# Optimization experiments

Hardware: AMD Instinct MI355X
Metric: run time of the kernel (lower is better)

Reference implementation:

```python
import jax, jax.numpy as jnp
import numpy as np

N_NODES = 50000
IN_CH = 128
OUT_CH = 64
HID = 2 * OUT_CH  # 128
N_EDGES = 800000


def _glorot(key, shape):
    fan_in, fan_out = shape[0], shape[-1]
    lim = jnp.sqrt(6.0 / (fan_in + fan_out))
    return jax.random.uniform(key, shape, jnp.float32, -lim, lim)


def setup_inputs() -> dict:
    key = jax.random.key(0)
    ks = jax.random.split(key, 10)
    x = jax.random.normal(ks[0], (N_NODES, IN_CH), jnp.float32)
    edge_index = jax.random.randint(ks[1], (2, N_EDGES), 0, N_NODES, jnp.int32)
    return {
        "x": x,
        "edge_index": edge_index,
        "W1": _glorot(ks[2], (IN_CH, HID)),
        "a_src1": _glorot(ks[3], (HID,)),
        "a_dst1": _glorot(ks[4], (HID,)),
        "b1": jnp.zeros((HID,), jnp.float32),
        "W2": _glorot(ks[5], (HID, OUT_CH)),
        "a_src2": _glorot(ks[6], (OUT_CH,)),
        "a_dst2": _glorot(ks[7], (OUT_CH,)),
        "b2": jnp.zeros((OUT_CH,), jnp.float32),
    }


def _gat_conv(x, src, dst, W, a_src, a_dst, b, n_nodes):
    # Linear transform: [N, F_out]
    h = x @ W
    # Per-node attention halves (heads=1): alpha_i = <h_i, a>
    al_s = h @ a_src  # [N]
    al_d = h @ a_dst  # [N]
    # Edge scores with LeakyReLU(0.2), PyG default negative slope
    e = jax.nn.leaky_relu(al_s[src] + al_d[dst], negative_slope=0.2)
    # Segment softmax over incoming edges of each dst node
    m = jax.ops.segment_max(e, dst, num_segments=n_nodes)
    m = jnp.where(jnp.isfinite(m), m, 0.0)
    ex = jnp.exp(e - m[dst])
    denom = jax.ops.segment_sum(ex, dst, num_segments=n_nodes)
    alpha = ex / (denom[dst] + 1e-16)  # [E]
    # Weighted scatter-add aggregation
    out = jax.ops.segment_sum(h[src] * alpha[:, None], dst, num_segments=n_nodes)
    return out + b


def reference(x, edge_index, W1, a_src1, a_dst1, b1, W2, a_src2, a_dst2, b2):
    n = x.shape[0]
    # add_self_loops=True (PyG GATConv default)
    loops = jnp.arange(n, dtype=edge_index.dtype)
    src = jnp.concatenate([edge_index[0], loops])
    dst = jnp.concatenate([edge_index[1], loops])
    h = _gat_conv(x.astype(jnp.float32), src, dst, W1, a_src1, a_dst1, b1, n)
    h = jax.nn.relu(h)
    return _gat_conv(h, src, dst, W2, a_src2, a_dst2, b2, n)
```

## Files before the change

### kernel.cpp

```cpp
#include <hip/hip_runtime.h>
#include <hip/hip_bf16.h>

#define N_NODES 50000
#define IN_CH 128
#define HID 128
#define OUT_CH 64
#define N_EDGES 800000
#define N_TOT_EDGES (N_EDGES + N_NODES)
#define ET_PAD (N_TOT_EDGES + 3 * N_NODES)
#define MPAD 50048
#define NBX (MPAD / 16)
#define NBN ((N_NODES + 255) / 256)

typedef float float4v __attribute__((ext_vector_type(4)));
typedef unsigned uint4v __attribute__((ext_vector_type(4)));
typedef __attribute__((ext_vector_type(8))) short bf16x8;
typedef __attribute__((ext_vector_type(4))) float f32x4;

__device__ __forceinline__ unsigned bf16_rne(float f) {
    unsigned u = __float_as_uint(f);
    return (u + 0x7fffu + ((u >> 16) & 1u)) >> 16;
}
__device__ __forceinline__ unsigned pack2(float a, float b) {
    return bf16_rne(a) | (bf16_rne(b) << 16);
}


__global__ void k_count(const int* __restrict__ dst_row, int* __restrict__ cnt,
                        unsigned short* __restrict__ rank, int e) {
    int i = blockIdx.x * 256 + threadIdx.x;
    if (i < e) {
        int d = __builtin_nontemporal_load(&dst_row[i]);
        rank[i] = (unsigned short)atomicAdd(&cnt[d], 1);
    }
}

__global__ void k_scan1(const int* __restrict__ cnt, int* __restrict__ off,
                        int* __restrict__ bsum, int n) {
    __shared__ int s[256];
    int t = threadIdx.x;
    int i = blockIdx.x * 256 + t;
    int v = (i < n) ? ((cnt[i] + 3) & ~3) : 0;
    s[t] = v;
    __syncthreads();
    for (int d = 1; d < 256; d <<= 1) {
        int x = (t >= d) ? s[t - d] : 0;
        __syncthreads();
        s[t] += x;
        __syncthreads();
    }
    if (i < n) off[i + 1] = s[t];
    if (t == 255) bsum[blockIdx.x] = s[255];
}

__global__ void k_scan2(int* __restrict__ bsum, int nb) {
    __shared__ int s[256];
    int t = threadIdx.x;
    int v = (t < nb) ? bsum[t] : 0;
    s[t] = v;
    __syncthreads();
    for (int d = 1; d < 256; d <<= 1) {
        int x = (t >= d) ? s[t - d] : 0;
        __syncthreads();
        s[t] += x;
        __syncthreads();
    }
    if (t < nb) bsum[t] = s[t] - v;
}

__global__ void k_scan3(int* __restrict__ off, const int* __restrict__ bsum, int n) {
    int i = blockIdx.x * 256 + threadIdx.x;
    if (i < n) off[i + 1] += bsum[blockIdx.x];
    if (i == 0) off[0] = 0;
}

__global__ void k_fill2(const int* __restrict__ ei, const int* __restrict__ off,
                        const unsigned short* __restrict__ rank,
                        int* __restrict__ csr, int e, int n) {
    int i = blockIdx.x * 256 + threadIdx.x;
    if (i < e) {
        int src = __builtin_nontemporal_load(&ei[i]);
        int dst = __builtin_nontemporal_load(&ei[e + i]);
        csr[off[dst] + rank[i]] = src;
    } else if (i < e + n) {
        int v = i - e;
        csr[off[v]] = v;
    }
}

__global__ __launch_bounds__(256) void k_cvtAll(
        const float* __restrict__ X, unsigned short* __restrict__ Xb,
        const float* __restrict__ W1, unsigned short* __restrict__ Wl1,
        const float* __restrict__ W2, unsigned short* __restrict__ Wl2,
        int* __restrict__ cnt, int M) {
    const int b = blockIdx.x;
    const int t = threadIdx.x;
    if (b < NBX) {
        const int kg = t >> 4, rl = t & 15;
        const int row = b * 16 + rl;
        float4 a = make_float4(0.f, 0.f, 0.f, 0.f), c = a;
        if (row < M) {
            a = *(const float4*)&X[(size_t)row * 128 + kg * 8];
            c = *(const float4*)&X[(size_t)row * 128 + kg * 8 + 4];
        }
        uint4 p;
        p.x = pack2(a.x, a.y); p.y = pack2(a.z, a.w);
        p.z = pack2(c.x, c.y); p.w = pack2(c.z, c.w);
        *(uint4*)&Xb[(size_t)b * 2048 + kg * 128 + rl * 8] = p;
        return;
    }
    if (b >= NBX + 12) {
        int i = (b - NBX - 12) * 256 + t;
        if (i < M) cnt[i] = 1;
        return;
    }
    const float* W; unsigned short* Wl; int N, bb;
    if (b < NBX + 8) { W = W1; Wl = Wl1; N = 128; bb = b - NBX; }
    else             { W = W2; Wl = Wl2; N = 64;  bb = b - NBX - 8; }
    const int tg = bb * 256 + t;
    if (tg >= 16 * N) return;
    const int kg = tg / N, col = tg & (N - 1);
    float v[8];
    #pragma unroll
    for (int j = 0; j < 8; ++j) v[j] = W[(size_t)(kg * 8 + j) * N + col];
    uint4 p;
    p.x = pack2(v[0], v[1]); p.y = pack2(v[2], v[3]);
    p.z = pack2(v[4], v[5]); p.w = pack2(v[6], v[7]);
    *(uint4*)&Wl[(size_t)tg * 8] = p;
}

template<int N>
__global__ __launch_bounds__(256) void gemm_mfma(
        const unsigned short* __restrict__ Xb, const unsigned short* __restrict__ Wlg,
        const float* __restrict__ asrc, const float* __restrict__ adst,
        unsigned short* __restrict__ Hb, float* __restrict__ als, float* __restrict__ ald,
        int M) {
    constexpr int NF = N / 16;
    __shared__ unsigned short Wl[16 * N * 8];
    const int t = threadIdx.x;
    for (int i = t; i < N * 16; i += 256)
        ((uint4*)Wl)[i] = ((const uint4*)Wlg)[i];
    __syncthreads();

    const int lane = t & 63, w = t >> 6;
    const int rb = blockIdx.x * 64 + w * 16;
    const int cl = lane & 15, g = lane >> 4;
    const unsigned short* __restrict__ Abase = Xb + (size_t)(rb >> 4) * 2048 + cl * 8;

    f32x4 acc[NF];
    #pragma unroll
    for (int n = 0; n < NF; ++n) acc[n] = (f32x4){0.f, 0.f, 0.f, 0.f};

    #pragma unroll
    for (int s = 0; s < 4; ++s) {
        bf16x8 af = *(const bf16x8*)(Abase + (s * 4 + g) * 128);
        #pragma unroll
        for (int n = 0; n < NF; ++n) {
            bf16x8 bf = *(const bf16x8*)(Wl + ((s * 4 + g) * N + n * 16 + cl) * 8);
            acc[n] = __builtin_amdgcn_mfma_f32_16x16x32_bf16(af, bf, acc[n], 0, 0, 0);
        }
    }

    float asv[NF], adv[NF];
    #pragma unroll
    for (int n = 0; n < NF; ++n) {
        asv[n] = asrc[n * 16 + cl];
        adv[n] = adst[n * 16 + cl];
    }

    #pragma unroll
    for (int r = 0; r < 4; ++r) {
        float ps = 0.f, pd = 0.f;
        #pragma unroll
        for (int n = 0; n < NF; ++n) {
            ps += acc[n][r] * asv[n];
            pd += acc[n][r] * adv[n];
        }
        #pragma unroll
        for (int mask = 1; mask < 16; mask <<= 1) {
            ps += __shfl_xor(ps, mask);
            pd += __shfl_xor(pd, mask);
        }
        const int row = rb + g * 4 + r;
        if (cl == 0 && row < M) { als[row] = ps; ald[row] = pd; }
    }

    #pragma unroll
    for (int r = 0; r < 4; ++r) {
        const int row = rb + g * 4 + r;
        if (row >= M) continue;
        #pragma unroll
        for (int n = 0; n < NF; ++n)
            Hb[(size_t)(n >> 1) * (size_t)M * 32 + (size_t)row * 32
               + (n & 1) * 16 + cl] = (unsigned short)bf16_rne(acc[n][r]);
    }
}

__global__ __launch_bounds__(256) void k_edgew(
        const float* __restrict__ als, const float* __restrict__ ald,
        const int* __restrict__ off, const int* __restrict__ cnt,
        const int* __restrict__ csr,
        unsigned* __restrict__ ew, float* __restrict__ invden, int n) {
    const int fl = threadIdx.x & 15;
    const int v = blockIdx.x * 16 + (threadIdx.x >> 4);
    if (v >= n) return;
    const int start = off[v], end = start + cnt[v];
    const int pend = off[v + 1];
    const float aldv = ald[v];
    float s = 0.f;
    for (int j = start + fl; j < end; j += 16) {
        int src = __builtin_nontemporal_load(&csr[j]);
        float e = als[src] + aldv;
        e = e > 0.f ? e : 0.2f * e;
        unsigned r = bf16_rne(__expf(e));
        ew[j] = ((unsigned)src << 16) | r;
        s += __uint_as_float(r << 16);
    }
    for (int j = end + fl; j < pend; j += 16) ew[j] = 0;
    #pragma unroll
    for (int d = 1; d < 16; d <<= 1) s += __shfl_xor(s, d);
    if (fl == 0) invden[v] = 1.f / (s + 1e-16f);
}

template<int F, bool RELU, bool PACKOUT>
__global__ __launch_bounds__(256) void k_spmm_b(
        const unsigned short* __restrict__ Hb, const unsigned* __restrict__ ew,
        const float* __restrict__ invden, const float* __restrict__ bias,
        const int* __restrict__ off, void* __restrict__ outv, int n) {
    constexpr int NCH = F / 32;
    const int chunk = blockIdx.x % NCH;
    const int v = (blockIdx.x / NCH) * 64 + (threadIdx.x >> 2);
    if (v >= n) return;
    const int q = threadIdx.x & 3;
    const int start = off[v], end = off[v + 1];
    const unsigned short* __restrict__ Hch = Hb + (size_t)chunk * (size_t)n * 32 + q * 8;

    float a0[8] = {}, a1[8] = {}, a2[8] = {}, a3[8] = {};

    #define GATB(E, A)                                                   \
        {                                                                \
            float w_ = __uint_as_float((E) << 16);                       \
            uint4 h_ = *(const uint4*)&Hch[(size_t)((E) >> 16) * 32];    \
            A[0] += w_ * __uint_as_float(h_.x << 16);                    \
            A[1] += w_ * __uint_as_float(h_.x & 0xffff0000u);            \
            A[2] += w_ * __uint_as_float(h_.y << 16);                    \
            A[3] += w_ * __uint_as_float(h_.y & 0xffff0000u);            \
            A[4] += w_ * __uint_as_float(h_.z << 16);                    \
            A[5] += w_ * __uint_as_float(h_.z & 0xffff0000u);            \
            A[6] += w_ * __uint_as_float(h_.w << 16);                    \
            A[7] += w_ * __uint_as_float(h_.w & 0xffff0000u);            \
        }
    #define GATB4(Q) GATB((Q).x, a0) GATB((Q).y, a1) GATB((Q).z, a2) GATB((Q).w, a3)

    int j = start;
    for (; j + 4 < end; j += 8) {
        uint4 eA = *(const uint4*)&ew[j];
        uint4 eB = *(const uint4*)&ew[j + 4];
        GATB4(eA)
        GATB4(eB)
    }
    if (j < end) {
        uint4 eA = *(const uint4*)&ew[j];
        GATB4(eA)
    }
    #undef GATB4
    #undef GATB

    const float inv = invden[v];
    const float* __restrict__ bp = bias + chunk * 32 + q * 8;
    float s[8];
    #pragma unroll
    for (int i = 0; i < 8; ++i) {
        s[i] = (a0[i] + a1[i] + a2[i] + a3[i]) * inv + bp[i];
        if (RELU) s[i] = fmaxf(s[i], 0.f);
    }

    if (PACKOUT) {
        unsigned short* Xb2 = (unsigned short*)outv;
        const int kg = chunk * 4 + q;
        uint4v p;
        p[0] = pack2(s[0], s[1]); p[1] = pack2(s[2], s[3]);
        p[2] = pack2(s[4], s[5]); p[3] = pack2(s[6], s[7]);
        __builtin_nontemporal_store(p,
            (uint4v*)&Xb2[(size_t)(v >> 4) * 2048 + kg * 128 + (v & 15) * 8]);
    } else {
        float* out = (float*)outv;
        float4v o0, o1;
        o0[0] = s[0]; o0[1] = s[1]; o0[2] = s[2]; o0[3] = s[3];
        o1[0] = s[4]; o1[1] = s[5]; o1[2] = s[6]; o1[3] = s[7];
        float* op = out + (size_t)v * F + chunk * 32 + q * 8;
        __builtin_nontemporal_store(o0, (float4v*)op);
        __builtin_nontemporal_store(o1, (float4v*)(op + 4));
    }
}


extern "C" void kernel_launch(void* const* d_in, const int* in_sizes, int n_in,
                              void* d_out, int out_size, void* d_ws, size_t ws_size,
                              hipStream_t stream) {
    const float* x     = (const float*)d_in[0];
    const int*   ei    = (const int*)d_in[1];
    const float* W1    = (const float*)d_in[2];
    const float* as1   = (const float*)d_in[3];
    const float* ad1   = (const float*)d_in[4];
    const float* b1    = (const float*)d_in[5];
    const float* W2    = (const float*)d_in[6];
    const float* as2   = (const float*)d_in[7];
    const float* ad2   = (const float*)d_in[8];
    const float* b2    = (const float*)d_in[9];
    float* out = (float*)d_out;

    const int Nn = N_NODES, E = N_EDGES, ET = N_TOT_EDGES;

    char* ws = (char*)d_ws;
    size_t o = 0;
    auto carve = [&](size_t bytes) { char* p = ws + o; o = (o + bytes + 255) & ~(size_t)255; return p; };
    int*            off  = (int*)carve((Nn + 1) * sizeof(int));
    int*            cnt  = (int*)carve(Nn * sizeof(int));
    int*            bsum = (int*)carve(256 * sizeof(int));
    unsigned short* rank = (unsigned short*)carve((size_t)E * sizeof(unsigned short));
    int*            csr  = (int*)carve((size_t)ET_PAD * sizeof(int));
    unsigned*       ew   = (unsigned*)carve((size_t)ET_PAD * sizeof(unsigned));
    unsigned short* h1b  = (unsigned short*)carve((size_t)Nn * HID * sizeof(unsigned short));
    unsigned short* h2b  = (unsigned short*)carve((size_t)Nn * OUT_CH * sizeof(unsigned short));
    unsigned short* Xb1  = (unsigned short*)carve((size_t)MPAD * 128 * sizeof(unsigned short));
    unsigned short* Xb2  = (unsigned short*)carve((size_t)MPAD * 128 * sizeof(unsigned short));
    unsigned short* Wl1  = (unsigned short*)carve(16 * 128 * 8 * sizeof(unsigned short));
    unsigned short* Wl2  = (unsigned short*)carve(16 * 64 * 8 * sizeof(unsigned short));
    float*          als  = (float*)carve(Nn * sizeof(float));
    float*          ald  = (float*)carve(Nn * sizeof(float));
    float*          invd = (float*)carve(Nn * sizeof(float));

    const int nbE   = (E + 255) / 256;
    const int nbET  = (ET + 255) / 256;

    k_cvtAll<<<NBX + 12 + NBN, 256, 0, stream>>>(x, Xb1, W1, Wl1, W2, Wl2, cnt, Nn);

    k_count<<<nbE, 256, 0, stream>>>(ei + E, cnt, rank, E);
    k_scan1<<<NBN, 256, 0, stream>>>(cnt, off, bsum, Nn);
    k_scan2<<<1, 256, 0, stream>>>(bsum, NBN);
    k_scan3<<<NBN, 256, 0, stream>>>(off, bsum, Nn);
    k_fill2<<<nbET, 256, 0, stream>>>(ei, off, rank, csr, E, Nn);

    const int nbEW   = (Nn + 15) / 16;
    const int nbN64  = (Nn + 63) / 64;
    const int nbGEMM = MPAD / 64;

    gemm_mfma<HID><<<nbGEMM, 256, 0, stream>>>(
        Xb1, Wl1, as1, ad1, h1b, als, ald, Nn);
    k_edgew<<<nbEW, 256, 0, stream>>>(als, ald, off, cnt, csr, ew, invd, Nn);
    k_spmm_b<HID, true, true><<<nbN64 * (HID / 32), 256, 0, stream>>>(
        h1b, ew, invd, b1, off, Xb2, Nn);

    gemm_mfma<OUT_CH><<<nbGEMM, 256, 0, stream>>>(
        Xb2, Wl2, as2, ad2, h2b, als, ald, Nn);
    k_edgew<<<nbEW, 256, 0, stream>>>(als, ald, off, cnt, csr, ew, invd, Nn);
    k_spmm_b<OUT_CH, false, false><<<nbN64 * (OUT_CH / 32), 256, 0, stream>>>(
        h2b, ew, invd, b2, off, out, Nn);
}
```

Before: 165.0 us.

## Fuse independent graph-build and GEMM kernels into shared grids, skip redundant pad zeroing

Merges the edge-count pass with the bf16 conversion pass, and the CSR fill pass with the layer-1 MFMA GEMM, into single kernels that dispatch on block index. Independent work can then overlap in one launch instead of serializing. The second edge-weight pass skips re-zeroing the padding slots because the first pass already zeroed them. The fused GEMM kernel always reserves the larger shared buffer, even for fill blocks, which may lower occupancy.

```diff
diff --git a/kernel.cpp b/kernel.cpp
--- a/kernel.cpp
+++ b/kernel.cpp
@@ -11,6 +11,10 @@
 #define MPAD 50048
 #define NBX (MPAD / 16)
 #define NBN ((N_NODES + 255) / 256)
+#define NB_E ((N_EDGES + 255) / 256)
+#define NB_ET ((N_TOT_EDGES + 255) / 256)
+#define NB_CVT (NBX + 12)
+#define NB_GEMM (MPAD / 64)
 
 typedef float float4v __attribute__((ext_vector_type(4)));
 typedef unsigned uint4v __attribute__((ext_vector_type(4)));
@@ -26,13 +30,144 @@
 }
 
 
-__global__ void k_count(const int* __restrict__ dst_row, int* __restrict__ cnt,
-                        unsigned short* __restrict__ rank, int e) {
-    int i = blockIdx.x * 256 + threadIdx.x;
+__device__ __forceinline__ void count_body(int b, int t,
+        const int* __restrict__ dst_row, int* __restrict__ cnt,
+        unsigned short* __restrict__ rank, int e) {
+    int i = b * 256 + t;
     if (i < e) {
         int d = __builtin_nontemporal_load(&dst_row[i]);
         rank[i] = (unsigned short)atomicAdd(&cnt[d], 1);
     }
+}
+
+__device__ __forceinline__ void cvt_body(int b, int t,
+        const float* __restrict__ X, unsigned short* __restrict__ Xb,
+        const float* __restrict__ W1, unsigned short* __restrict__ Wl1,
+        const float* __restrict__ W2, unsigned short* __restrict__ Wl2, int M) {
+    if (b < NBX) {
+        const int kg = t >> 4, rl = t & 15;
+        const int row = b * 16 + rl;
+        float4 a = make_float4(0.f, 0.f, 0.f, 0.f), c = a;
+        if (row < M) {
+            a = *(const float4*)&X[(size_t)row * 128 + kg * 8];
+            c = *(const float4*)&X[(size_t)row * 128 + kg * 8 + 4];
+        }
+        uint4 p;
+        p.x = pack2(a.x, a.y); p.y = pack2(a.z, a.w);
+        p.z = pack2(c.x, c.y); p.w = pack2(c.z, c.w);
+        *(uint4*)&Xb[(size_t)b * 2048 + kg * 128 + rl * 8] = p;
+        return;
+    }
+    const float* W; unsigned short* Wl; int N, bb;
+    if (b < NBX + 8) { W = W1; Wl = Wl1; N = 128; bb = b - NBX; }
+    else             { W = W2; Wl = Wl2; N = 64;  bb = b - NBX - 8; }
+    const int tg = bb * 256 + t;
+    if (tg >= 16 * N) return;
+    const int kg = tg / N, col = tg & (N - 1);
+    float v[8];
+    #pragma unroll
+    for (int j = 0; j < 8; ++j) v[j] = W[(size_t)(kg * 8 + j) * N + col];
+    uint4 p;
+    p.x = pack2(v[0], v[1]); p.y = pack2(v[2], v[3]);
+    p.z = pack2(v[4], v[5]); p.w = pack2(v[6], v[7]);
+    *(uint4*)&Wl[(size_t)tg * 8] = p;
+}
+
+__device__ __forceinline__ void fill_body(int b, int t,
+        const int* __restrict__ ei, const int* __restrict__ off,
+        const unsigned short* __restrict__ rank,
+        int* __restrict__ csr, int e, int n) {
+    int i = b * 256 + t;
+    if (i < e) {
+        int src = __builtin_nontemporal_load(&ei[i]);
+        int dst = __builtin_nontemporal_load(&ei[e + i]);
+        csr[off[dst] + rank[i]] = src;
+    } else if (i < e + n) {
+        int v = i - e;
+        csr[off[v]] = v;
+    }
+}
+
+template<int N>
+__device__ __forceinline__ void gemm_body(int gb, int t,
+        const unsigned short* __restrict__ Xb, const unsigned short* __restrict__ Wlg,
+        const float* __restrict__ asrc, const float* __restrict__ adst,
+        unsigned short* __restrict__ Hb, float* __restrict__ als,
+        float* __restrict__ ald, int M, unsigned short* Wl) {
+    constexpr int NF = N / 16;
+    for (int i = t; i < N * 16; i += 256)
+        ((uint4*)Wl)[i] = ((const uint4*)Wlg)[i];
+    __syncthreads();
+
+    const int lane = t & 63, w = t >> 6;
+    const int rb = gb * 64 + w * 16;
+    const int cl = lane & 15, g = lane >> 4;
+    const unsigned short* __restrict__ Abase = Xb + (size_t)(rb >> 4) * 2048 + cl * 8;
+
+    f32x4 acc[NF];
+    #pragma unroll
+    for (int n = 0; n < NF; ++n) acc[n] = (f32x4){0.f, 0.f, 0.f, 0.f};
+
+    #pragma unroll
+    for (int s = 0; s < 4; ++s) {
+        bf16x8 af = *(const bf16x8*)(Abase + (s * 4 + g) * 128);
+        #pragma unroll
+        for (int n = 0; n < NF; ++n) {
+            bf16x8 bf = *(const bf16x8*)(Wl + ((s * 4 + g) * N + n * 16 + cl) * 8);
+            acc[n] = __builtin_amdgcn_mfma_f32_16x16x32_bf16(af, bf, acc[n], 0, 0, 0);
+        }
+    }
+
+    float asv[NF], adv[NF];
+    #pragma unroll
+    for (int n = 0; n < NF; ++n) {
+        asv[n] = asrc[n * 16 + cl];
+        adv[n] = adst[n * 16 + cl];
+    }
+
+    #pragma unroll
+    for (int r = 0; r < 4; ++r) {
+        float ps = 0.f, pd = 0.f;
+        #pragma unroll
+        for (int n = 0; n < NF; ++n) {
+            ps += acc[n][r] * asv[n];
+            pd += acc[n][r] * adv[n];
+        }
+        #pragma unroll
+        for (int mask = 1; mask < 16; mask <<= 1) {
+            ps += __shfl_xor(ps, mask);
+            pd += __shfl_xor(pd, mask);
+        }
+        const int row = rb + g * 4 + r;
+        if (cl == 0 && row < M) { als[row] = ps; ald[row] = pd; }
+    }
+
+    #pragma unroll
+    for (int r = 0; r < 4; ++r) {
+        const int row = rb + g * 4 + r;
+        if (row >= M) continue;
+        #pragma unroll
+        for (int n = 0; n < NF; ++n)
+            Hb[(size_t)(n >> 1) * (size_t)M * 32 + (size_t)row * 32
+               + (n & 1) * 16 + cl] = (unsigned short)bf16_rne(acc[n][r]);
+    }
+}
+
+
+__global__ void k_init_cnt(int* cnt, int n) {
+    int i = blockIdx.x * 256 + threadIdx.x;
+    if (i < n) cnt[i] = 1;
+}
+
+__global__ __launch_bounds__(256) void k_par1(
+        const int* __restrict__ ei, int* __restrict__ cnt,
+        unsigned short* __restrict__ rank,
+        const float* __restrict__ X, unsigned short* __restrict__ Xb,
+        const float* __restrict__ W1, unsigned short* __restrict__ Wl1,
+        const float* __restrict__ W2, unsigned short* __restrict__ Wl2, int M) {
+    const int b = blockIdx.x, t = threadIdx.x;
+    if (b < NB_E) count_body(b, t, ei + N_EDGES, cnt, rank, N_EDGES);
+    else         cvt_body(b - NB_E, t, X, Xb, W1, Wl1, W2, Wl2, M);
 }
 
 __global__ void k_scan1(const int* __restrict__ cnt, int* __restrict__ off,
@@ -74,128 +209,29 @@
     if (i == 0) off[0] = 0;
 }
 
-__global__ void k_fill2(const int* __restrict__ ei, const int* __restrict__ off,
-                        const unsigned short* __restrict__ rank,
-                        int* __restrict__ csr, int e, int n) {
-    int i = blockIdx.x * 256 + threadIdx.x;
-    if (i < e) {
-        int src = __builtin_nontemporal_load(&ei[i]);
-        int dst = __builtin_nontemporal_load(&ei[e + i]);
-        csr[off[dst] + rank[i]] = src;
-    } else if (i < e + n) {
-        int v = i - e;
-        csr[off[v]] = v;
-    }
-}
-
-__global__ __launch_bounds__(256) void k_cvtAll(
-        const float* __restrict__ X, unsigned short* __restrict__ Xb,
-        const float* __restrict__ W1, unsigned short* __restrict__ Wl1,
-        const float* __restrict__ W2, unsigned short* __restrict__ Wl2,
-        int* __restrict__ cnt, int M) {
-    const int b = blockIdx.x;
-    const int t = threadIdx.x;
-    if (b < NBX) {
-        const int kg = t >> 4, rl = t & 15;
-        const int row = b * 16 + rl;
-        float4 a = make_float4(0.f, 0.f, 0.f, 0.f), c = a;
-        if (row < M) {
-            a = *(const float4*)&X[(size_t)row * 128 + kg * 8];
-            c = *(const float4*)&X[(size_t)row * 128 + kg * 8 + 4];
-        }
-        uint4 p;
-        p.x = pack2(a.x, a.y); p.y = pack2(a.z, a.w);
-        p.z = pack2(c.x, c.y); p.w = pack2(c.z, c.w);
-        *(uint4*)&Xb[(size_t)b * 2048 + kg * 128 + rl * 8] = p;
-        return;
-    }
-    if (b >= NBX + 12) {
-        int i = (b - NBX - 12) * 256 + t;
-        if (i < M) cnt[i] = 1;
-        return;
-    }
-    const float* W; unsigned short* Wl; int N, bb;
-    if (b < NBX + 8) { W = W1; Wl = Wl1; N = 128; bb = b - NBX; }
-    else             { W = W2; Wl = Wl2; N = 64;  bb = b - NBX - 8; }
-    const int tg = bb * 256 + t;
-    if (tg >= 16 * N) return;
-    const int kg = tg / N, col = tg & (N - 1);
-    float v[8];
-    #pragma unroll
-    for (int j = 0; j < 8; ++j) v[j] = W[(size_t)(kg * 8 + j) * N + col];
-    uint4 p;
-    p.x = pack2(v[0], v[1]); p.y = pack2(v[2], v[3]);
-    p.z = pack2(v[4], v[5]); p.w = pack2(v[6], v[7]);
-    *(uint4*)&Wl[(size_t)tg * 8] = p;
-}
-
-template<int N>
-__global__ __launch_bounds__(256) void gemm_mfma(
+__global__ __launch_bounds__(256) void k_par2(
+        const int* __restrict__ ei, const int* __restrict__ off,
+        const unsigned short* __restrict__ rank, int* __restrict__ csr,
         const unsigned short* __restrict__ Xb, const unsigned short* __restrict__ Wlg,
         const float* __restrict__ asrc, const float* __restrict__ adst,
-        unsigned short* __restrict__ Hb, float* __restrict__ als, float* __restrict__ ald,
-        int M) {
-    constexpr int NF = N / 16;
-    __shared__ unsigned short Wl[16 * N * 8];
-    const int t = threadIdx.x;
-    for (int i = t; i < N * 16; i += 256)
-        ((uint4*)Wl)[i] = ((const uint4*)Wlg)[i];
-    __syncthreads();
-
-    const int lane = t & 63, w = t >> 6;
-    const int rb = blockIdx.x * 64 + w * 16;
-    const int cl = lane & 15, g = lane >> 4;
-    const unsigned short* __restrict__ Abase = Xb + (size_t)(rb >> 4) * 2048 + cl * 8;
-
-    f32x4 acc[NF];
-    #pragma unroll
-    for (int n = 0; n < NF; ++n) acc[n] = (f32x4){0.f, 0.f, 0.f, 0.f};
-
-    #pragma unroll
-    for (int s = 0; s < 4; ++s) {
-        bf16x8 af = *(const bf16x8*)(Abase + (s * 4 + g) * 128);
-        #pragma unroll
-        for (int n = 0; n < NF; ++n) {
-            bf16x8 bf = *(const bf16x8*)(Wl + ((s * 4 + g) * N + n * 16 + cl) * 8);
-            acc[n] = __builtin_amdgcn_mfma_f32_16x16x32_bf16(af, bf, acc[n], 0, 0, 0);
-        }
-    }
-
-    float asv[NF], adv[NF];
-    #pragma unroll
-    for (int n = 0; n < NF; ++n) {
-        asv[n] = asrc[n * 16 + cl];
-        adv[n] = adst[n * 16 + cl];
-    }
-
-    #pragma unroll
-    for (int r = 0; r < 4; ++r) {
-        float ps = 0.f, pd = 0.f;
-        #pragma unroll
-        for (int n = 0; n < NF; ++n) {
-            ps += acc[n][r] * asv[n];
-            pd += acc[n][r] * adv[n];
-        }
-        #pragma unroll
-        for (int mask = 1; mask < 16; mask <<= 1) {
-            ps += __shfl_xor(ps, mask);
-            pd += __shfl_xor(pd, mask);
-        }
-        const int row = rb + g * 4 + r;
-        if (cl == 0 && row < M) { als[row] = ps; ald[row] = pd; }
-    }
-
-    #pragma unroll
-    for (int r = 0; r < 4; ++r) {
-        const int row = rb + g * 4 + r;
-        if (row >= M) continue;
-        #pragma unroll
-        for (int n = 0; n < NF; ++n)
-            Hb[(size_t)(n >> 1) * (size_t)M * 32 + (size_t)row * 32
-               + (n & 1) * 16 + cl] = (unsigned short)bf16_rne(acc[n][r]);
-    }
-}
-
+        unsigned short* __restrict__ Hb, float* __restrict__ als,
+        float* __restrict__ ald, int M) {
+    __shared__ unsigned short Wl[16 * 128 * 8];
+    const int b = blockIdx.x, t = threadIdx.x;
+    if (b < NB_ET) fill_body(b, t, ei, off, rank, csr, N_EDGES, N_NODES);
+    else gemm_body<HID>(b - NB_ET, t, Xb, Wlg, asrc, adst, Hb, als, ald, M, Wl);
+}
+
+__global__ __launch_bounds__(256) void gemm_mfma64(
+        const unsigned short* __restrict__ Xb, const unsigned short* __restrict__ Wlg,
+        const float* __restrict__ asrc, const float* __restrict__ adst,
+        unsigned short* __restrict__ Hb, float* __restrict__ als,
+        float* __restrict__ ald, int M) {
+    __shared__ unsigned short Wl[16 * 64 * 8];
+    gemm_body<OUT_CH>(blockIdx.x, threadIdx.x, Xb, Wlg, asrc, adst, Hb, als, ald, M, Wl);
+}
+
+template<bool PADZ>
 __global__ __launch_bounds__(256) void k_edgew(
         const float* __restrict__ als, const float* __restrict__ ald,
         const int* __restrict__ off, const int* __restrict__ cnt,
@@ -205,7 +241,6 @@
     const int v = blockIdx.x * 16 + (threadIdx.x >> 4);
     if (v >= n) return;
     const int start = off[v], end = start + cnt[v];
-    const int pend = off[v + 1];
     const float aldv = ald[v];
     float s = 0.f;
     for (int j = start + fl; j < end; j += 16) {
@@ -216,7 +251,10 @@
         ew[j] = ((unsigned)src << 16) | r;
         s += __uint_as_float(r << 16);
     }
-    for (int j = end + fl; j < pend; j += 16) ew[j] = 0;
+    if (PADZ) {
+        const int pend = off[v + 1];
+        for (int j = end + fl; j < pend; j += 16) ew[j] = 0;
+    }
     #pragma unroll
     for (int d = 1; d < 16; d <<= 1) s += __shfl_xor(s, d);
     if (fl == 0) invden[v] = 1.f / (s + 1e-16f);
@@ -310,7 +348,7 @@
     const float* b2    = (const float*)d_in[9];
     float* out = (float*)d_out;
 
-    const int Nn = N_NODES, E = N_EDGES, ET = N_TOT_EDGES;
+    const int Nn = N_NODES;
 
     char* ws = (char*)d_ws;
     size_t o = 0;
@@ -318,7 +356,7 @@
     int*            off  = (int*)carve((Nn + 1) * sizeof(int));
     int*            cnt  = (int*)carve(Nn * sizeof(int));
     int*            bsum = (int*)carve(256 * sizeof(int));
-    unsigned short* rank = (unsigned short*)carve((size_t)E * sizeof(unsigned short));
+    unsigned short* rank = (unsigned short*)carve((size_t)N_EDGES * sizeof(unsigned short));
     int*            csr  = (int*)carve((size_t)ET_PAD * sizeof(int));
     unsigned*       ew   = (unsigned*)carve((size_t)ET_PAD * sizeof(unsigned));
     unsigned short* h1b  = (unsigned short*)carve((size_t)Nn * HID * sizeof(unsigned short));
@@ -331,30 +369,28 @@
     float*          ald  = (float*)carve(Nn * sizeof(float));
     float*          invd = (float*)carve(Nn * sizeof(float));
 
-    const int nbE   = (E + 255) / 256;
-    const int nbET  = (ET + 255) / 256;
-
-    k_cvtAll<<<NBX + 12 + NBN, 256, 0, stream>>>(x, Xb1, W1, Wl1, W2, Wl2, cnt, Nn);
-
-    k_count<<<nbE, 256, 0, stream>>>(ei + E, cnt, rank, E);
+    k_init_cnt<<<NBN, 256, 0, stream>>>(cnt, Nn);
+
+    k_par1<<<NB_E + NB_CVT, 256, 0, stream>>>(
+        ei, cnt, rank, x, Xb1, W1, Wl1, W2, Wl2, Nn);
+
     k_scan1<<<NBN, 256, 0, stream>>>(cnt, off, bsum, Nn);
     k_scan2<<<1, 256, 0, stream>>>(bsum, NBN);
     k_scan3<<<NBN, 256, 0, stream>>>(off, bsum, Nn);
-    k_fill2<<<nbET, 256, 0, stream>>>(ei, off, rank, csr, E, Nn);
-
-    const int nbEW   = (Nn + 15) / 16;
-    const int nbN64  = (Nn + 63) / 64;
-    const int nbGEMM = MPAD / 64;
-
-    gemm_mfma<HID><<<nbGEMM, 256, 0, stream>>>(
-        Xb1, Wl1, as1, ad1, h1b, als, ald, Nn);
-    k_edgew<<<nbEW, 256, 0, stream>>>(als, ald, off, cnt, csr, ew, invd, Nn);
+
+    k_par2<<<NB_ET + NB_GEMM, 256, 0, stream>>>(
+        ei, off, rank, csr, Xb1, Wl1, as1, ad1, h1b, als, ald, Nn);
+
+    const int nbEW  = (Nn + 15) / 16;
+    const int nbN64 = (Nn + 63) / 64;
+
+    k_edgew<true><<<nbEW, 256, 0, stream>>>(als, ald, off, cnt, csr, ew, invd, Nn);
     k_spmm_b<HID, true, true><<<nbN64 * (HID / 32), 256, 0, stream>>>(
         h1b, ew, invd, b1, off, Xb2, Nn);
 
-    gemm_mfma<OUT_CH><<<nbGEMM, 256, 0, stream>>>(
+    gemm_mfma64<<<NB_GEMM, 256, 0, stream>>>(
         Xb2, Wl2, as2, ad2, h2b, als, ald, Nn);
-    k_edgew<<<nbEW, 256, 0, stream>>>(als, ald, off, cnt, csr, ew, invd, Nn);
+    k_edgew<false><<<nbEW, 256, 0, stream>>>(als, ald, off, cnt, csr, ew, invd, Nn);
     k_spmm_b<OUT_CH, false, false><<<nbN64 * (OUT_CH / 32), 256, 0, stream>>>(
         h2b, ew, invd, b2, off, out, Nn);
 }
```

Result: no change. 162.7 us (-1.4%).
